# Kernel optimization log

Measured on AMD Instinct MI355X. Metric: run time of the kernel, lower is better.

Reference implementation:

```python
import jax, jax.numpy as jnp
import numpy as np

D = 768      # feature_dim
HD = 768     # hidden_dim
NH = 4       # num_heads
B, T1, T2 = 4, 128, 128
LN_EPS = 1e-5

def setup_inputs() -> dict:
    key = jax.random.key(0)
    ks = jax.random.split(key, 12)
    s = 0.02
    return {
        'speech_features': jax.random.normal(ks[0], (B, T1, D), jnp.float32),
        'phoneme_features': jax.random.normal(ks[1], (B, T2, D), jnp.float32),
        # per-head attention MLP: Linear(2D->HD), ReLU, Linear(HD->1); stacked over heads
        'W1': jax.random.normal(ks[2], (NH, 2 * D, HD), jnp.float32) * s,
        'b1': jnp.zeros((NH, HD), jnp.float32),
        'w2': jax.random.normal(ks[3], (NH, HD), jnp.float32) * s,
        'b2': jnp.zeros((NH,), jnp.float32),
        # fusion: Linear(2D->2HD), ReLU, Linear(2HD->D), LayerNorm(D)
        'Wf1': jax.random.normal(ks[4], (2 * D, 2 * HD), jnp.float32) * s,
        'bf1': jnp.zeros((2 * HD,), jnp.float32),
        'Wf2': jax.random.normal(ks[5], (2 * HD, D), jnp.float32) * s,
        'bf2': jnp.zeros((D,), jnp.float32),
        'ln_g': jnp.ones((D,), jnp.float32),
        'ln_b': jnp.zeros((D,), jnp.float32),
    }

def reference(speech_features, phoneme_features, W1, b1, w2, b2, Wf1, bf1, Wf2, bf2, ln_g, ln_b):
    d = speech_features.shape[-1]
    # Decompose Linear(cat([speech_t, phoneme])) = speech@W1[:d] + phoneme@W1[d:] + b1
    Wx, Wy = W1[:, :d, :], W1[:, d:, :]
    sx = jnp.einsum('btd,ndh->nbth', speech_features, Wx)   # [NH,B,T1,HD]
    py = jnp.einsum('bsd,ndh->nbsh', phoneme_features, Wy)  # [NH,B,T2,HD]
    hidden = jax.nn.relu(sx[:, :, :, None, :] + py[:, :, None, :, :]
                         + b1[:, None, None, None, :])      # [NH,B,T1,T2,HD]
    scores = jnp.einsum('nbtsh,nh->nbts', hidden, w2) + b2[:, None, None, None]
    attn = jax.nn.softmax(scores, axis=-1).mean(axis=0)     # [B,T1,T2]
    context = jnp.einsum('bts,bsd->btd', attn, phoneme_features)  # [B,T1,D]
    fused = jnp.concatenate([speech_features, context], axis=-1)  # [B,T1,2D]
    # dropout is identity in eval mode
    h = jax.nn.relu(fused @ Wf1 + bf1)
    out = h @ Wf2 + bf2
    mu = out.mean(axis=-1, keepdims=True)
    var = ((out - mu) ** 2).mean(axis=-1, keepdims=True)
    out = (out - mu) * jax.lax.rsqrt(var + LN_EPS) * ln_g + ln_b
    return out.mean(axis=1)  # [B,D]
```

## Files before the change

### kernel.cpp

```cpp
#include <hip/hip_runtime.h>
#include <cstddef>


#define D_  768
#define HD_ 768
#define NH_ 4
#define B_  4
#define T1_ 128
#define T2_ 128
#define M_  (B_*T1_)
#define LN_EPS_ 1e-5f

typedef unsigned short u16;
typedef unsigned int u32;
typedef _Float16 f16;
typedef _Float16 f16x2 __attribute__((ext_vector_type(2)));
typedef __bf16 bf16x8 __attribute__((ext_vector_type(8)));
typedef float f32x4 __attribute__((ext_vector_type(4)));

__device__ __forceinline__ u16 f2bf(float f) {
    union { float f; unsigned int u; } v; v.f = f;
    unsigned int u = v.u + (0x7FFFu + ((v.u >> 16) & 1u));
    return (u16)(u >> 16);
}
__device__ __forceinline__ u16 f16bits(f16 h) {
    return __builtin_bit_cast(unsigned short, h);
}
__device__ __forceinline__ f16x2 bcast2(u32 u) {
    return __builtin_bit_cast(f16x2, u);
}
__device__ __forceinline__ u32 splat2(u16 h) { return (u32)h * 0x10001u; }

template<bool RELU, int MODE>
__device__ __forceinline__ void gemm_mfma_body(
    const u16* __restrict__ A, int lda,
    const u16* __restrict__ Bt, int ldb,
    const float* __restrict__ bias,
    void* __restrict__ C, int ldc, int K, int m0, int n0)
{
    __shared__ __align__(16) u16 As[64][40];
    __shared__ __align__(16) u16 Bs[64][40];
    __shared__ u16 Ts[MODE == 3 ? 64 : 1][MODE == 3 ? 68 : 1];

    const int tid = threadIdx.x;
    const int row = tid >> 2;
    const int kq  = (tid & 3) << 3;
    const int lane = tid & 63;
    const int w  = tid >> 6;
    const int wr = (w >> 1) << 5;
    const int wc = (w & 1) << 5;
    const int l16 = lane & 15;
    const int lk8 = (lane >> 4) << 3;
    const int r4  = (lane >> 4) << 2;

    const u16* aptr = A + (size_t)(m0 + row) * lda + kq;
    const u16* bptr = Bt + (size_t)(n0 + row) * ldb + kq;

    f32x4 acc00 = {0.f,0.f,0.f,0.f}, acc01 = {0.f,0.f,0.f,0.f};
    f32x4 acc10 = {0.f,0.f,0.f,0.f}, acc11 = {0.f,0.f,0.f,0.f};

    uint4 a_nxt = *(const uint4*)aptr;
    uint4 b_nxt = *(const uint4*)bptr;

    for (int k0 = 0; k0 < K; k0 += 32) {
        __syncthreads();
        *(uint4*)&As[row][kq] = a_nxt;
        *(uint4*)&Bs[row][kq] = b_nxt;
        if (k0 + 32 < K) {
            a_nxt = *(const uint4*)(aptr + k0 + 32);
            b_nxt = *(const uint4*)(bptr + k0 + 32);
        }
        __syncthreads();
        bf16x8 af0 = *(const bf16x8*)&As[wr + l16][lk8];
        bf16x8 af1 = *(const bf16x8*)&As[wr + 16 + l16][lk8];
        bf16x8 bf0 = *(const bf16x8*)&Bs[wc + l16][lk8];
        bf16x8 bf1 = *(const bf16x8*)&Bs[wc + 16 + l16][lk8];
        acc00 = __builtin_amdgcn_mfma_f32_16x16x32_bf16(af0, bf0, acc00, 0, 0, 0);
        acc01 = __builtin_amdgcn_mfma_f32_16x16x32_bf16(af0, bf1, acc01, 0, 0, 0);
        acc10 = __builtin_amdgcn_mfma_f32_16x16x32_bf16(af1, bf0, acc10, 0, 0, 0);
        acc11 = __builtin_amdgcn_mfma_f32_16x16x32_bf16(af1, bf1, acc11, 0, 0, 0);
    }

#define EPI_FRAG(ACC, MF, NF)                                                  \
    {                                                                          \
        const int gcol = n0 + wc + (NF)*16 + l16;                              \
        const float bv = bias ? bias[gcol] : 0.f;                              \
        float v_[4];                                                           \
        _Pragma("unroll")                                                      \
        for (int r = 0; r < 4; r++) {                                          \
            float v = ACC[r] + bv;                                             \
            if (RELU) v = fmaxf(v, 0.f);                                       \
            v_[r] = v;                                                         \
        }                                                                      \
        const int lr0 = wr + (MF)*16 + r4;                                     \
        if (MODE == 3) {                                                       \
            const int lc = wc + (NF)*16 + l16;                                 \
            _Pragma("unroll")                                                  \
            for (int r = 0; r < 4; r++) Ts[lc][lr0 + r] = f16bits((f16)v_[r]); \
        } else {                                                               \
            _Pragma("unroll")                                                  \
            for (int r = 0; r < 4; r++) {                                      \
                const size_t off = (size_t)(m0 + lr0 + r) * ldc + gcol;        \
                if (MODE == 0) ((float*)C)[off] = v_[r];                       \
                else if (MODE == 1) ((u16*)C)[off] = f2bf(v_[r]);              \
                else ((u16*)C)[off] = f16bits((f16)v_[r]);                     \
            }                                                                  \
        }                                                                      \
    }
    EPI_FRAG(acc00, 0, 0) EPI_FRAG(acc01, 0, 1)
    EPI_FRAG(acc10, 1, 0) EPI_FRAG(acc11, 1, 1)
#undef EPI_FRAG

    if (MODE == 3) {
        __syncthreads();
        u16* cb = (u16*)C + (size_t)(m0 >> 7) * (768 * 128) + (m0 & 127);
#pragma unroll
        for (int u = 0; u < 4; u++) {
            const int i = tid + u * 256;
            const int hl = i >> 4;
            const int s4 = (i & 15) << 2;
            ushort4 o;
            o.x = Ts[hl][s4 + 0]; o.y = Ts[hl][s4 + 1];
            o.z = Ts[hl][s4 + 2]; o.w = Ts[hl][s4 + 3];
            *(ushort4*)(cb + (size_t)(n0 + hl) * 128 + s4) = o;
        }
    }
}

__global__ __launch_bounds__(256) void prep_kernel(
    const float* __restrict__ speech, const float* __restrict__ phon,
    const float* __restrict__ W1, const float* __restrict__ Wf1,
    const float* __restrict__ Wf2,
    u16* __restrict__ spb, u16* __restrict__ phb,
    u16* __restrict__ w1t, u16* __restrict__ wf1t, u16* __restrict__ wf2t)
{
    const int tid = threadIdx.x;
    int bid = blockIdx.x;
    if (bid < 768) {
        const bool isp = bid < 384;
        const float* in = isp ? speech : phon;
        u16* outb = isp ? spb : phb;
        const int i = ((isp ? bid : bid - 384) * 256 + tid) * 4;
        float4 v = *(const float4*)(in + i);
        ushort4 o;
        o.x = f2bf(v.x); o.y = f2bf(v.y); o.z = f2bf(v.z); o.w = f2bf(v.w);
        *(ushort4*)(outb + i) = o;
        return;
    }
    bid -= 768;
    const float* in; u16* outp; int tx, ty;
    if (bid < 4608) {
        const int z = bid / 1152, r = bid % 1152;
        tx = r % 24; ty = r / 24;
        in = W1 + (size_t)z * 1536 * 768; outp = w1t + (size_t)z * 768 * 1536;
    } else if (bid < 6912) {
        const int r = bid - 4608;
        tx = r % 48; ty = r / 48;
        in = Wf1; outp = wf1t;
    } else {
        const int r = bid - 6912;
        tx = r % 24; ty = r / 24;
        in = Wf2; outp = wf2t;
    }
    const int C = (bid >= 4608 && bid < 6912) ? 1536 : 768;
    const int c0 = tx * 32, r0 = ty * 32;
    __shared__ float tile[32][33];
    const int tr = tid >> 3, tc = (tid & 7) << 2;
    float4 v = *(const float4*)(in + (size_t)(r0 + tr) * C + c0 + tc);
    tile[tr][tc] = v.x; tile[tr][tc + 1] = v.y;
    tile[tr][tc + 2] = v.z; tile[tr][tc + 3] = v.w;
    __syncthreads();
    ushort4 o;
    o.x = f2bf(tile[tc + 0][tr]); o.y = f2bf(tile[tc + 1][tr]);
    o.z = f2bf(tile[tc + 2][tr]); o.w = f2bf(tile[tc + 3][tr]);
    *(ushort4*)(outp + (size_t)(c0 + tr) * 1536 + r0 + tc) = o;
}

__global__ __launch_bounds__(256) void gemm_sxpy_kernel(
    const u16* __restrict__ sp, const u16* __restrict__ ph,
    const u16* __restrict__ w1t, const float* __restrict__ b1,
    u16* __restrict__ sxf, u16* __restrict__ pyt)
{
    const int z = blockIdx.z;
    const int n = z & 3;
    const bool ispy = z >= 4;
    const u16* Bt = w1t + (size_t)n * 768 * 1536 + (ispy ? 768 : 0);
    if (!ispy) {
        gemm_mfma_body<false, 2>(sp, 768, Bt, 1536, b1 + n * HD_,
                                 sxf + (size_t)n * M_ * HD_, HD_, 768,
                                 blockIdx.y * 64, blockIdx.x * 64);
    } else {
        gemm_mfma_body<false, 3>(ph, 768, Bt, 1536, nullptr,
                                 pyt + (size_t)n * 4 * 768 * 128, 0, 768,
                                 blockIdx.y * 64, blockIdx.x * 64);
    }
}

template<bool RELU, int MODE>
__global__ __launch_bounds__(256) void gemm_mfma_kernel(
    const u16* __restrict__ A, int lda,
    const u16* __restrict__ Bt, int ldb,
    const float* __restrict__ bias,
    void* __restrict__ C, int ldc, int K)
{
    gemm_mfma_body<RELU, MODE>(A, lda, Bt, ldb, bias, C, ldc, K,
                               blockIdx.y * 64, blockIdx.x * 64);
}

__global__ __launch_bounds__(256) void scores_softmax_kernel(
    const u16* __restrict__ sxf,
    const u16* __restrict__ pyt,
    const float* __restrict__ w2,
    float* __restrict__ probs)
{
    const int bid = blockIdx.x;
    const int n = bid >> 7, b = (bid >> 5) & 3, t0 = (bid & 31) * 4;
    const int tid = threadIdx.x, lane = tid & 63, w = tid >> 6;

    __shared__ __align__(16) f16x2 sxs[4][768];
    __shared__ __align__(16) f16x2 w2s[768];

#pragma unroll
    for (int q = 0; q < 3; q++) {
        const int u = tid + q * 256;
        const int r = u / 192;
        const int h4 = (u % 192) * 4;
        ushort4 v = *(const ushort4*)(sxf + ((size_t)(n * 512 + b * 128 + t0 + r)) * 768 + h4);
        sxs[r][h4 + 0] = bcast2(splat2(v.x));
        sxs[r][h4 + 1] = bcast2(splat2(v.y));
        sxs[r][h4 + 2] = bcast2(splat2(v.z));
        sxs[r][h4 + 3] = bcast2(splat2(v.w));
    }
#pragma unroll
    for (int q = 0; q < 3; q++) {
        const int i = tid + q * 256;
        w2s[i] = bcast2(splat2(f16bits((f16)w2[n * 768 + i])));
    }
    __syncthreads();

    const f16x2* pypanel = (const f16x2*)(pyt + ((size_t)((n << 2) | b)) * 768 * 128) + lane;
    const f16x2 z2 = {(f16)0, (f16)0};

    float acc0 = 0.f, acc1 = 0.f;

    f16x2 b0[16], b1[16];
#pragma unroll
    for (int j = 0; j < 16; j++) b0[j] = pypanel[(size_t)j * 64];
#pragma unroll
    for (int j = 0; j < 16; j++) b1[j] = pypanel[(size_t)(16 + j) * 64];

    for (int hc = 0; hc < 768; hc += 32) {
        f16x2 a4[4] = {z2, z2, z2, z2};
#pragma unroll
        for (int j = 0; j < 16; j++) {
            f16x2 r_ = __builtin_elementwise_max(sxs[w][hc + j] + b0[j], z2);
            a4[j & 3] = __builtin_elementwise_fma(r_, w2s[hc + j], a4[j & 3]);
        }
        if (hc + 32 < 768) {
#pragma unroll
            for (int j = 0; j < 16; j++) b0[j] = pypanel[(size_t)(hc + 32 + j) * 64];
        }
#pragma unroll
        for (int j = 0; j < 16; j++) {
            f16x2 r_ = __builtin_elementwise_max(sxs[w][hc + 16 + j] + b1[j], z2);
            a4[j & 3] = __builtin_elementwise_fma(r_, w2s[hc + 16 + j], a4[j & 3]);
        }
        if (hc + 48 < 768) {
#pragma unroll
            for (int j = 0; j < 16; j++) b1[j] = pypanel[(size_t)(hc + 48 + j) * 64];
        }
#pragma unroll
        for (int k = 0; k < 4; k++) {
            acc0 += (float)a4[k].x;
            acc1 += (float)a4[k].y;
        }
    }

    float mx = fmaxf(acc0, acc1);
#pragma unroll
    for (int off = 32; off; off >>= 1) mx = fmaxf(mx, __shfl_xor(mx, off, 64));
    const float e0 = expf(acc0 - mx), e1 = expf(acc1 - mx);
    float sm = e0 + e1;
#pragma unroll
    for (int off = 32; off; off >>= 1) sm += __shfl_xor(sm, off, 64);
    const float inv = 0.25f / sm;
    float2 pr; pr.x = e0 * inv; pr.y = e1 * inv;
    *(float2*)&probs[((size_t)(n * 512 + b * 128 + t0 + w)) * 128 + 2 * lane] = pr;
}

__global__ __launch_bounds__(256) void context_fused_kernel(
    const float* __restrict__ probs, const float* __restrict__ phon,
    const float* __restrict__ speech, u16* __restrict__ fused)
{
    const int m = blockIdx.x;
    const int b = m >> 7;
    const int tid = threadIdx.x;
    __shared__ float attn[T2_];
    if (tid < T2_) {
        float a = 0.f;
#pragma unroll
        for (int n = 0; n < NH_; n++)
            a += probs[(size_t)(n * M_ + m) * T2_ + tid];
        attn[tid] = a;
    }
    __syncthreads();
    const float* ph = phon + (size_t)b * T2_ * D_;
#pragma unroll
    for (int j = 0; j < 3; j++) {
        const int d = tid + 256 * j;
        float acc = 0.f;
#pragma unroll 8
        for (int s = 0; s < T2_; s++)
            acc = fmaf(attn[s], ph[(size_t)s * D_ + d], acc);
        fused[(size_t)m * (2 * D_) + d] = f2bf(speech[(size_t)m * D_ + d]);
        fused[(size_t)m * (2 * D_) + D_ + d] = f2bf(acc);
    }
}

__global__ __launch_bounds__(256) void ln_fused_kernel(
    const float* __restrict__ x, const float* __restrict__ g,
    const float* __restrict__ lb, float* __restrict__ out)
{
    const int b = blockIdx.x, tid = threadIdx.x, lane = tid & 63, w = tid >> 6;
    __shared__ float rs[T1_];
    __shared__ float Sred[4];

    float prsum = 0.f;
    for (int i = 0; i < 32; i++) {
        const int row = w * 32 + i;
        const float4* x4 = (const float4*)(x + ((size_t)(b * T1_ + row)) * D_);
        float s = 0.f, ss = 0.f;
#pragma unroll
        for (int j = 0; j < 3; j++) {
            float4 v = x4[j * 64 + lane];
            s += v.x + v.y + v.z + v.w;
            ss += v.x * v.x + v.y * v.y + v.z * v.z + v.w * v.w;
        }
#pragma unroll
        for (int off = 32; off; off >>= 1) {
            s += __shfl_xor(s, off, 64);
            ss += __shfl_xor(ss, off, 64);
        }
        if (lane == 0) {
            const float mu = s * (1.f / D_);
            const float var = ss * (1.f / D_) - mu * mu;
            const float r = rsqrtf(var + LN_EPS_);
            rs[row] = r;
            prsum += mu * r;
        }
    }
    if (lane == 0) Sred[w] = prsum;
    __syncthreads();
    const float S = Sred[0] + Sred[1] + Sred[2] + Sred[3];
    const float* xb = x + (size_t)b * T1_ * D_;
#pragma unroll
    for (int j = 0; j < 3; j++) {
        const int d = tid + 256 * j;
        float acc = 0.f;
#pragma unroll 8
        for (int t = 0; t < T1_; t++)
            acc = fmaf(xb[(size_t)t * D_ + d], rs[t], acc);
        out[b * D_ + d] = g[d] * (acc - S) * (1.f / T1_) + lb[d];
    }
}

extern "C" void kernel_launch(void* const* d_in, const int* in_sizes, int n_in,
                              void* d_out, int out_size, void* d_ws, size_t ws_size,
                              hipStream_t stream)
{
    const float* speech = (const float*)d_in[0];
    const float* phon   = (const float*)d_in[1];
    const float* W1     = (const float*)d_in[2];
    const float* b1     = (const float*)d_in[3];
    const float* w2     = (const float*)d_in[4];
    const float* Wf1    = (const float*)d_in[6];
    const float* bf1    = (const float*)d_in[7];
    const float* Wf2    = (const float*)d_in[8];
    const float* bf2    = (const float*)d_in[9];
    const float* ln_g   = (const float*)d_in[10];
    const float* ln_b   = (const float*)d_in[11];
    float* out = (float*)d_out;

    char* w = (char*)d_ws;
    auto alloc = [&](size_t bytes) { char* p = w; w += (bytes + 1023) & ~(size_t)1023; return p; };
    u16* sp_bf  = (u16*)alloc((size_t)M_ * D_ * 2);
    u16* ph_bf  = (u16*)alloc((size_t)M_ * D_ * 2);
    u16* w1t    = (u16*)alloc((size_t)NH_ * 768 * 1536 * 2);
    u16* wf1t   = (u16*)alloc((size_t)1536 * 1536 * 2);
    u16* wf2t   = (u16*)alloc((size_t)768 * 1536 * 2);
    u16* sxf    = (u16*)alloc((size_t)NH_ * M_ * HD_ * 2);
    u16* pyt    = (u16*)alloc((size_t)NH_ * B_ * 768 * 128 * 2);
    float* probs  = (float*)alloc((size_t)NH_ * M_ * T2_ * 4);
    u16* fusedb = (u16*)alloc((size_t)M_ * 2 * D_ * 2);
    u16* hbuf   = (u16*)alloc((size_t)M_ * 2 * HD_ * 2);
    float* outpre = (float*)alloc((size_t)M_ * D_ * 4);

    hipLaunchKernelGGL(prep_kernel, dim3(8832), dim3(256), 0, stream,
                       speech, phon, W1, Wf1, Wf2, sp_bf, ph_bf, w1t, wf1t, wf2t);
    hipLaunchKernelGGL(gemm_sxpy_kernel, dim3(HD_ / 64, M_ / 64, 8), dim3(256), 0, stream,
                       sp_bf, ph_bf, w1t, b1, sxf, pyt);
    hipLaunchKernelGGL(scores_softmax_kernel, dim3(512), dim3(256), 0, stream,
                       sxf, pyt, w2, probs);
    hipLaunchKernelGGL(context_fused_kernel, dim3(M_), dim3(256), 0, stream,
                       probs, phon, speech, fusedb);
    hipLaunchKernelGGL((gemm_mfma_kernel<true, 1>), dim3(2 * HD_ / 64, M_ / 64), dim3(256), 0, stream,
                       fusedb, 2 * D_, wf1t, 1536, bf1, hbuf, 2 * HD_, 2 * D_);
    hipLaunchKernelGGL((gemm_mfma_kernel<false, 0>), dim3(D_ / 64, M_ / 64), dim3(256), 0, stream,
                       hbuf, 2 * HD_, wf2t, 1536, bf2, outpre, D_, 2 * HD_);
    hipLaunchKernelGGL(ln_fused_kernel, dim3(B_), dim3(256), 0, stream,
                       outpre, ln_g, ln_b, out);
}
```

Baseline: 134.8 us.

## Fuse fp32-to-bf16 activation conversion into GEMM loads and retile score kernel

The GEMMs now read fp32 activations directly and convert them to bf16 during the A-tile load. This removes the separate activation conversion in the prep kernel and the bf16 fused-concat buffer, and the FFN1 GEMM reads speech and context through split pointers. The scores kernel handles 8 query rows per block, two per wave, so each pyt load is reused across two rows, and the LayerNorm-mean kernel is split across 12 blocks instead of 4. The cost is wider fp32 A loads inside the GEMM inner loop, a separate fp32 context buffer, and fewer blocks in the scores kernel.

```diff
diff --git a/kernel.cpp b/kernel.cpp
--- a/kernel.cpp
+++ b/kernel.cpp
@@ -23,6 +23,9 @@
     unsigned int u = v.u + (0x7FFFu + ((v.u >> 16) & 1u));
     return (u16)(u >> 16);
 }
+__device__ __forceinline__ u32 pack_bf2(float lo, float hi) {
+    return (u32)f2bf(lo) | ((u32)f2bf(hi) << 16);
+}
 __device__ __forceinline__ u16 f16bits(f16 h) {
     return __builtin_bit_cast(unsigned short, h);
 }
@@ -31,9 +34,9 @@
 }
 __device__ __forceinline__ u32 splat2(u16 h) { return (u32)h * 0x10001u; }
 
-template<bool RELU, int MODE>
+template<bool RELU, int MODE, bool AF32, bool SPLIT>
 __device__ __forceinline__ void gemm_mfma_body(
-    const u16* __restrict__ A, int lda,
+    const void* __restrict__ Av1, const void* __restrict__ Av2, int lda,
     const u16* __restrict__ Bt, int ldb,
     const float* __restrict__ bias,
     void* __restrict__ C, int ldc, int K, int m0, int n0)
@@ -53,13 +56,30 @@
     const int lk8 = (lane >> 4) << 3;
     const int r4  = (lane >> 4) << 2;
 
-    const u16* aptr = A + (size_t)(m0 + row) * lda + kq;
-    const u16* bptr = Bt + (size_t)(n0 + row) * ldb + kq;
+    const u16*   aptr16  = (const u16*)Av1 + (size_t)(m0 + row) * lda + kq;
+    const float* aptrf1  = (const float*)Av1 + (size_t)(m0 + row) * lda + kq;
+    const float* aptrf2  = SPLIT ? ((const float*)Av2 + (size_t)(m0 + row) * lda + kq) : nullptr;
+    const u16*   bptr    = Bt + (size_t)(n0 + row) * ldb + kq;
 
     f32x4 acc00 = {0.f,0.f,0.f,0.f}, acc01 = {0.f,0.f,0.f,0.f};
     f32x4 acc10 = {0.f,0.f,0.f,0.f}, acc11 = {0.f,0.f,0.f,0.f};
 
-    uint4 a_nxt = *(const uint4*)aptr;
+    auto loadA = [&](int k0) -> uint4 {
+        if (AF32) {
+            const float* base = aptrf1;
+            int kk = k0;
+            if (SPLIT && k0 >= 768) { base = aptrf2; kk = k0 - 768; }
+            float4 ax = *(const float4*)(base + kk);
+            float4 ay = *(const float4*)(base + kk + 4);
+            uint4 r;
+            r.x = pack_bf2(ax.x, ax.y); r.y = pack_bf2(ax.z, ax.w);
+            r.z = pack_bf2(ay.x, ay.y); r.w = pack_bf2(ay.z, ay.w);
+            return r;
+        }
+        return *(const uint4*)(aptr16 + k0);
+    };
+
+    uint4 a_nxt = loadA(0);
     uint4 b_nxt = *(const uint4*)bptr;
 
     for (int k0 = 0; k0 < K; k0 += 32) {
@@ -67,7 +87,7 @@
         *(uint4*)&As[row][kq] = a_nxt;
         *(uint4*)&Bs[row][kq] = b_nxt;
         if (k0 + 32 < K) {
-            a_nxt = *(const uint4*)(aptr + k0 + 32);
+            a_nxt = loadA(k0 + 32);
             b_nxt = *(const uint4*)(bptr + k0 + 32);
         }
         __syncthreads();
@@ -128,26 +148,12 @@
 }
 
 __global__ __launch_bounds__(256) void prep_kernel(
-    const float* __restrict__ speech, const float* __restrict__ phon,
     const float* __restrict__ W1, const float* __restrict__ Wf1,
     const float* __restrict__ Wf2,
-    u16* __restrict__ spb, u16* __restrict__ phb,
     u16* __restrict__ w1t, u16* __restrict__ wf1t, u16* __restrict__ wf2t)
 {
     const int tid = threadIdx.x;
     int bid = blockIdx.x;
-    if (bid < 768) {
-        const bool isp = bid < 384;
-        const float* in = isp ? speech : phon;
-        u16* outb = isp ? spb : phb;
-        const int i = ((isp ? bid : bid - 384) * 256 + tid) * 4;
-        float4 v = *(const float4*)(in + i);
-        ushort4 o;
-        o.x = f2bf(v.x); o.y = f2bf(v.y); o.z = f2bf(v.z); o.w = f2bf(v.w);
-        *(ushort4*)(outb + i) = o;
-        return;
-    }
-    bid -= 768;
     const float* in; u16* outp; int tx, ty;
     if (bid < 4608) {
         const int z = bid / 1152, r = bid % 1152;
@@ -177,7 +183,7 @@
 }
 
 __global__ __launch_bounds__(256) void gemm_sxpy_kernel(
-    const u16* __restrict__ sp, const u16* __restrict__ ph,
+    const float* __restrict__ sp, const float* __restrict__ ph,
     const u16* __restrict__ w1t, const float* __restrict__ b1,
     u16* __restrict__ sxf, u16* __restrict__ pyt)
 {
@@ -186,25 +192,33 @@
     const bool ispy = z >= 4;
     const u16* Bt = w1t + (size_t)n * 768 * 1536 + (ispy ? 768 : 0);
     if (!ispy) {
-        gemm_mfma_body<false, 2>(sp, 768, Bt, 1536, b1 + n * HD_,
-                                 sxf + (size_t)n * M_ * HD_, HD_, 768,
-                                 blockIdx.y * 64, blockIdx.x * 64);
+        gemm_mfma_body<false, 2, true, false>(sp, nullptr, 768, Bt, 1536, b1 + n * HD_,
+                                              sxf + (size_t)n * M_ * HD_, HD_, 768,
+                                              blockIdx.y * 64, blockIdx.x * 64);
     } else {
-        gemm_mfma_body<false, 3>(ph, 768, Bt, 1536, nullptr,
-                                 pyt + (size_t)n * 4 * 768 * 128, 0, 768,
-                                 blockIdx.y * 64, blockIdx.x * 64);
-    }
-}
-
-template<bool RELU, int MODE>
-__global__ __launch_bounds__(256) void gemm_mfma_kernel(
-    const u16* __restrict__ A, int lda,
-    const u16* __restrict__ Bt, int ldb,
-    const float* __restrict__ bias,
-    void* __restrict__ C, int ldc, int K)
-{
-    gemm_mfma_body<RELU, MODE>(A, lda, Bt, ldb, bias, C, ldc, K,
-                               blockIdx.y * 64, blockIdx.x * 64);
+        gemm_mfma_body<false, 3, true, false>(ph, nullptr, 768, Bt, 1536, nullptr,
+                                              pyt + (size_t)n * 4 * 768 * 128, 0, 768,
+                                              blockIdx.y * 64, blockIdx.x * 64);
+    }
+}
+
+__global__ __launch_bounds__(256) void gemm_ffn1_kernel(
+    const float* __restrict__ speech, const float* __restrict__ ctx,
+    const u16* __restrict__ wf1t, const float* __restrict__ bf1,
+    u16* __restrict__ hbuf)
+{
+    gemm_mfma_body<true, 1, true, true>(speech, ctx, 768, wf1t, 1536, bf1,
+                                        hbuf, 1536, 1536,
+                                        blockIdx.y * 64, blockIdx.x * 64);
+}
+
+__global__ __launch_bounds__(256) void gemm_ffn2_kernel(
+    const u16* __restrict__ hbuf, const u16* __restrict__ wf2t,
+    const float* __restrict__ bf2, float* __restrict__ outpre)
+{
+    gemm_mfma_body<false, 0, false, false>(hbuf, nullptr, 1536, wf2t, 1536, bf2,
+                                           outpre, 768, 1536,
+                                           blockIdx.y * 64, blockIdx.x * 64);
 }
 
 __global__ __launch_bounds__(256) void scores_softmax_kernel(
@@ -214,14 +228,13 @@
     float* __restrict__ probs)
 {
     const int bid = blockIdx.x;
-    const int n = bid >> 7, b = (bid >> 5) & 3, t0 = (bid & 31) * 4;
+    const int n = bid >> 6, b = (bid >> 4) & 3, t0 = (bid & 15) * 8;
     const int tid = threadIdx.x, lane = tid & 63, w = tid >> 6;
 
-    __shared__ __align__(16) f16x2 sxs[4][768];
+    __shared__ __align__(16) f16x2 sxs[8][768];
     __shared__ __align__(16) f16x2 w2s[768];
 
-#pragma unroll
-    for (int q = 0; q < 3; q++) {
+    for (int q = 0; q < 6; q++) {
         const int u = tid + q * 256;
         const int r = u / 192;
         const int h4 = (u % 192) * 4;
@@ -231,7 +244,6 @@
         sxs[r][h4 + 2] = bcast2(splat2(v.z));
         sxs[r][h4 + 3] = bcast2(splat2(v.w));
     }
-#pragma unroll
     for (int q = 0; q < 3; q++) {
         const int i = tid + q * 256;
         w2s[i] = bcast2(splat2(f16bits((f16)w2[n * 768 + i])));
@@ -241,7 +253,8 @@
     const f16x2* pypanel = (const f16x2*)(pyt + ((size_t)((n << 2) | b)) * 768 * 128) + lane;
     const f16x2 z2 = {(f16)0, (f16)0};
 
-    float acc0 = 0.f, acc1 = 0.f;
+    float accA0 = 0.f, accA1 = 0.f, accB0 = 0.f, accB1 = 0.f;
+    const int rA = 2 * w, rB = 2 * w + 1;
 
     f16x2 b0[16], b1[16];
 #pragma unroll
@@ -249,48 +262,64 @@
 #pragma unroll
     for (int j = 0; j < 16; j++) b1[j] = pypanel[(size_t)(16 + j) * 64];
 
+    auto compute = [&](const f16x2 (&buf)[16], int hbase) {
+        f16x2 aA = z2, aB = z2;
+#pragma unroll
+        for (int j4 = 0; j4 < 16; j4 += 4) {
+            uint4 sau = *(const uint4*)&sxs[rA][hbase + j4];
+            uint4 sbu = *(const uint4*)&sxs[rB][hbase + j4];
+            uint4 wvu = *(const uint4*)&w2s[hbase + j4];
+            const u32 sa_[4] = {sau.x, sau.y, sau.z, sau.w};
+            const u32 sb_[4] = {sbu.x, sbu.y, sbu.z, sbu.w};
+            const u32 wv_[4] = {wvu.x, wvu.y, wvu.z, wvu.w};
+#pragma unroll
+            for (int j = 0; j < 4; j++) {
+                const f16x2 pv = buf[j4 + j];
+                const f16x2 wj = bcast2(wv_[j]);
+                f16x2 ra = __builtin_elementwise_max(bcast2(sa_[j]) + pv, z2);
+                f16x2 rb = __builtin_elementwise_max(bcast2(sb_[j]) + pv, z2);
+                aA = __builtin_elementwise_fma(ra, wj, aA);
+                aB = __builtin_elementwise_fma(rb, wj, aB);
+            }
+        }
+        accA0 += (float)aA.x; accA1 += (float)aA.y;
+        accB0 += (float)aB.x; accB1 += (float)aB.y;
+    };
+
     for (int hc = 0; hc < 768; hc += 32) {
-        f16x2 a4[4] = {z2, z2, z2, z2};
-#pragma unroll
-        for (int j = 0; j < 16; j++) {
-            f16x2 r_ = __builtin_elementwise_max(sxs[w][hc + j] + b0[j], z2);
-            a4[j & 3] = __builtin_elementwise_fma(r_, w2s[hc + j], a4[j & 3]);
-        }
+        compute(b0, hc);
         if (hc + 32 < 768) {
 #pragma unroll
             for (int j = 0; j < 16; j++) b0[j] = pypanel[(size_t)(hc + 32 + j) * 64];
         }
-#pragma unroll
-        for (int j = 0; j < 16; j++) {
-            f16x2 r_ = __builtin_elementwise_max(sxs[w][hc + 16 + j] + b1[j], z2);
-            a4[j & 3] = __builtin_elementwise_fma(r_, w2s[hc + 16 + j], a4[j & 3]);
-        }
+        compute(b1, hc + 16);
         if (hc + 48 < 768) {
 #pragma unroll
             for (int j = 0; j < 16; j++) b1[j] = pypanel[(size_t)(hc + 48 + j) * 64];
         }
-#pragma unroll
-        for (int k = 0; k < 4; k++) {
-            acc0 += (float)a4[k].x;
-            acc1 += (float)a4[k].y;
-        }
-    }
-
-    float mx = fmaxf(acc0, acc1);
-#pragma unroll
-    for (int off = 32; off; off >>= 1) mx = fmaxf(mx, __shfl_xor(mx, off, 64));
-    const float e0 = expf(acc0 - mx), e1 = expf(acc1 - mx);
-    float sm = e0 + e1;
-#pragma unroll
-    for (int off = 32; off; off >>= 1) sm += __shfl_xor(sm, off, 64);
-    const float inv = 0.25f / sm;
-    float2 pr; pr.x = e0 * inv; pr.y = e1 * inv;
-    *(float2*)&probs[((size_t)(n * 512 + b * 128 + t0 + w)) * 128 + 2 * lane] = pr;
-}
-
-__global__ __launch_bounds__(256) void context_fused_kernel(
+    }
+
+#pragma unroll
+    for (int which = 0; which < 2; which++) {
+        const float s0 = which ? accB0 : accA0;
+        const float s1 = which ? accB1 : accA1;
+        const int t = t0 + 2 * w + which;
+        float mx = fmaxf(s0, s1);
+#pragma unroll
+        for (int off = 32; off; off >>= 1) mx = fmaxf(mx, __shfl_xor(mx, off, 64));
+        const float e0 = expf(s0 - mx), e1 = expf(s1 - mx);
+        float sm = e0 + e1;
+#pragma unroll
+        for (int off = 32; off; off >>= 1) sm += __shfl_xor(sm, off, 64);
+        const float inv = 0.25f / sm;
+        float2 pr; pr.x = e0 * inv; pr.y = e1 * inv;
+        *(float2*)&probs[((size_t)(n * 512 + b * 128 + t)) * 128 + 2 * lane] = pr;
+    }
+}
+
+__global__ __launch_bounds__(256) void context_kernel(
     const float* __restrict__ probs, const float* __restrict__ phon,
-    const float* __restrict__ speech, u16* __restrict__ fused)
+    float* __restrict__ ctx)
 {
     const int m = blockIdx.x;
     const int b = m >> 7;
@@ -312,8 +341,7 @@
 #pragma unroll 8
         for (int s = 0; s < T2_; s++)
             acc = fmaf(attn[s], ph[(size_t)s * D_ + d], acc);
-        fused[(size_t)m * (2 * D_) + d] = f2bf(speech[(size_t)m * D_ + d]);
-        fused[(size_t)m * (2 * D_) + D_ + d] = f2bf(acc);
+        ctx[(size_t)m * D_ + d] = acc;
     }
 }
 
@@ -321,7 +349,8 @@
     const float* __restrict__ x, const float* __restrict__ g,
     const float* __restrict__ lb, float* __restrict__ out)
 {
-    const int b = blockIdx.x, tid = threadIdx.x, lane = tid & 63, w = tid >> 6;
+    const int b = blockIdx.x / 3, c = blockIdx.x % 3;
+    const int tid = threadIdx.x, lane = tid & 63, w = tid >> 6;
     __shared__ float rs[T1_];
     __shared__ float Sred[4];
 
@@ -353,15 +382,12 @@
     __syncthreads();
     const float S = Sred[0] + Sred[1] + Sred[2] + Sred[3];
     const float* xb = x + (size_t)b * T1_ * D_;
-#pragma unroll
-    for (int j = 0; j < 3; j++) {
-        const int d = tid + 256 * j;
-        float acc = 0.f;
+    const int d = c * 256 + tid;
+    float acc = 0.f;
 #pragma unroll 8
-        for (int t = 0; t < T1_; t++)
-            acc = fmaf(xb[(size_t)t * D_ + d], rs[t], acc);
-        out[b * D_ + d] = g[d] * (acc - S) * (1.f / T1_) + lb[d];
-    }
+    for (int t = 0; t < T1_; t++)
+        acc = fmaf(xb[(size_t)t * D_ + d], rs[t], acc);
+    out[b * D_ + d] = g[d] * (acc - S) * (1.f / T1_) + lb[d];
 }
 
 extern "C" void kernel_launch(void* const* d_in, const int* in_sizes, int n_in,
@@ -383,30 +409,28 @@
 
     char* w = (char*)d_ws;
     auto alloc = [&](size_t bytes) { char* p = w; w += (bytes + 1023) & ~(size_t)1023; return p; };
-    u16* sp_bf  = (u16*)alloc((size_t)M_ * D_ * 2);
-    u16* ph_bf  = (u16*)alloc((size_t)M_ * D_ * 2);
     u16* w1t    = (u16*)alloc((size_t)NH_ * 768 * 1536 * 2);
     u16* wf1t   = (u16*)alloc((size_t)1536 * 1536 * 2);
     u16* wf2t   = (u16*)alloc((size_t)768 * 1536 * 2);
     u16* sxf    = (u16*)alloc((size_t)NH_ * M_ * HD_ * 2);
     u16* pyt    = (u16*)alloc((size_t)NH_ * B_ * 768 * 128 * 2);
     float* probs  = (float*)alloc((size_t)NH_ * M_ * T2_ * 4);
-    u16* fusedb = (u16*)alloc((size_t)M_ * 2 * D_ * 2);
+    float* ctxb   = (float*)alloc((size_t)M_ * D_ * 4);
     u16* hbuf   = (u16*)alloc((size_t)M_ * 2 * HD_ * 2);
     float* outpre = (float*)alloc((size_t)M_ * D_ * 4);
 
-    hipLaunchKernelGGL(prep_kernel, dim3(8832), dim3(256), 0, stream,
-                       speech, phon, W1, Wf1, Wf2, sp_bf, ph_bf, w1t, wf1t, wf2t);
+    hipLaunchKernelGGL(prep_kernel, dim3(8064), dim3(256), 0, stream,
+                       W1, Wf1, Wf2, w1t, wf1t, wf2t);
     hipLaunchKernelGGL(gemm_sxpy_kernel, dim3(HD_ / 64, M_ / 64, 8), dim3(256), 0, stream,
-                       sp_bf, ph_bf, w1t, b1, sxf, pyt);
-    hipLaunchKernelGGL(scores_softmax_kernel, dim3(512), dim3(256), 0, stream,
+                       speech, phon, w1t, b1, sxf, pyt);
+    hipLaunchKernelGGL(scores_softmax_kernel, dim3(256), dim3(256), 0, stream,
                        sxf, pyt, w2, probs);
-    hipLaunchKernelGGL(context_fused_kernel, dim3(M_), dim3(256), 0, stream,
-                       probs, phon, speech, fusedb);
-    hipLaunchKernelGGL((gemm_mfma_kernel<true, 1>), dim3(2 * HD_ / 64, M_ / 64), dim3(256), 0, stream,
-                       fusedb, 2 * D_, wf1t, 1536, bf1, hbuf, 2 * HD_, 2 * D_);
-    hipLaunchKernelGGL((gemm_mfma_kernel<false, 0>), dim3(D_ / 64, M_ / 64), dim3(256), 0, stream,
-                       hbuf, 2 * HD_, wf2t, 1536, bf2, outpre, D_, 2 * HD_);
-    hipLaunchKernelGGL(ln_fused_kernel, dim3(B_), dim3(256), 0, stream,
+    hipLaunchKernelGGL(context_kernel, dim3(M_), dim3(256), 0, stream,
+                       probs, phon, ctxb);
+    hipLaunchKernelGGL(gemm_ffn1_kernel, dim3(2 * HD_ / 64, M_ / 64), dim3(256), 0, stream,
+                       speech, ctxb, wf1t, bf1, hbuf);
+    hipLaunchKernelGGL(gemm_ffn2_kernel, dim3(D_ / 64, M_ / 64), dim3(256), 0, stream,
+                       hbuf, wf2t, bf2, outpre);
+    hipLaunchKernelGGL(ln_fused_kernel, dim3(12), dim3(256), 0, stream,
                        outpre, ln_g, ln_b, out);
 }
```

Measured after the change: 142.6 us. 1.06x slower.
